# Performance work log

Measured on AMD Instinct MI355X. Metric: run time of the kernel, lower is better.

Reference implementation:

```python
import jax, jax.numpy as jnp
import numpy as np


def setup_inputs() -> dict:
    key = jax.random.key(0)
    k0, k1, k2, k3 = jax.random.split(key, 4)
    B, S, D, F, E = 2, 2048, 1024, 4096, 8
    scale = 0.02
    return {
        "x": jax.random.normal(k0, (B, S, D), jnp.float32),
        "gate_w": jax.random.normal(k1, (E, D), jnp.float32) * scale,
        "gate_b": jnp.zeros((E,), jnp.float32),
        "w1": jax.random.normal(k2, (E, D, F), jnp.float32) * scale,
        "b1": jnp.zeros((E, F), jnp.float32),
        "w2": jax.random.normal(k3, (E, F, D), jnp.float32) * scale,
        "b2": jnp.zeros((E, D), jnp.float32),
        "top_k": 2,
    }


def reference(x, gate_w, gate_b, w1, b1, w2, b2, top_k):
    B, S, D = x.shape
    E = gate_w.shape[0]
    xt = x.reshape(-1, D)                                   # [T, D]
    T = xt.shape[0]

    # Router: softmax over gate logits, then top-k and renormalize.
    gate_probs = jax.nn.softmax(xt @ gate_w.T + gate_b, axis=-1)   # [T, E]
    weights, selected = jax.lax.top_k(gate_probs, top_k)           # [T, k]
    weights = weights / jnp.sum(weights, axis=-1, keepdims=True)

    # Per-token combine weights over experts (zero where not selected),
    # equivalent to the per-expert gather/scatter loop in the original.
    combine = jnp.zeros((T, E), x.dtype).at[
        jnp.arange(T)[:, None], selected
    ].add(weights)                                                 # [T, E]

    # Expert MLPs (dense over experts, masked combine).
    h = jax.nn.silu(jnp.einsum("td,edf->etf", xt, w1) + b1[:, None, :])  # [E, T, F]
    expert_out = jnp.einsum("etf,efd->etd", h, w2) + b2[:, None, :]      # [E, T, D]
    out = jnp.einsum("etd,te->td", expert_out, combine)                  # [T, D]
    return out.reshape(B, S, D)
```

## Files before the change

kernel.cpp:

```cpp
#include <hip/hip_runtime.h>

#define T_TOK 4096
#define DIM   1024
#define FDIM  4096
#define NEXP  8

typedef __bf16 bf16x8 __attribute__((ext_vector_type(8)));
typedef __bf16 bf16x4 __attribute__((ext_vector_type(4)));
typedef float  f32x4  __attribute__((ext_vector_type(4)));
typedef const __attribute__((address_space(3))) char* lds3;

__device__ __forceinline__ void glds16(const void* g, void* l) {
    __builtin_amdgcn_global_load_lds(
        (const __attribute__((address_space(1))) void*)g,
        (__attribute__((address_space(3))) void*)l, 16, 0, 0);
}

#define DSR(dst, a, imm) \
    asm volatile("ds_read_b128 %0, %1 offset:" #imm : "=v"(dst) : "v"(a))

__device__ __forceinline__ int xcd_swz(int phys, int total) {
    int q = total >> 3, r = total & 7;
    int x = phys & 7, i = phys >> 3;
    return (x < r ? x * (q + 1) : r * (q + 1) + (x - r) * q) + i;
}

__global__ __launch_bounds__(64)
void moe_router(const float* __restrict__ x,
                const float* __restrict__ gw,
                const float* __restrict__ gb,
                const int*   __restrict__ topk_p,
                int*   __restrict__ counts,
                int*   __restrict__ bucket,
                float* __restrict__ bweight,
                __bf16* __restrict__ xb) {
    const int t = blockIdx.x;
    const int lane = threadIdx.x;
    float part[NEXP];
#pragma unroll
    for (int e = 0; e < NEXP; ++e) part[e] = 0.f;
    const float* xrow = x + (size_t)t * DIM;
    __bf16* xbrow = xb + (size_t)t * DIM;
#pragma unroll
    for (int r = 0; r < 4; ++r) {
        int c = r * 256 + lane * 4;
        float4 v = *(const float4*)&xrow[c];
        bf16x4 o; o[0]=(__bf16)v.x; o[1]=(__bf16)v.y; o[2]=(__bf16)v.z; o[3]=(__bf16)v.w;
        *(bf16x4*)&xbrow[c] = o;
#pragma unroll
        for (int e = 0; e < NEXP; ++e) {
            float4 g = *(const float4*)&gw[e * DIM + c];
            part[e] += v.x*g.x + v.y*g.y + v.z*g.z + v.w*g.w;
        }
    }
#pragma unroll
    for (int off = 32; off > 0; off >>= 1) {
#pragma unroll
        for (int e = 0; e < NEXP; ++e) part[e] += __shfl_xor(part[e], off);
    }
    if (lane == 0) {
        int k = topk_p[0];
        if (k < 1) k = 1;
        if (k > NEXP) k = NEXP;
        float p[NEXP];
        float mx = -1e30f;
#pragma unroll
        for (int e = 0; e < NEXP; ++e) {
            p[e] = part[e] + gb[e];
            mx = fmaxf(mx, p[e]);
        }
#pragma unroll
        for (int e = 0; e < NEXP; ++e) p[e] = __expf(p[e] - mx);
        bool used[NEXP];
#pragma unroll
        for (int e = 0; e < NEXP; ++e) used[e] = false;
        int sel[NEXP]; float selp[NEXP]; float wsum = 0.f;
        for (int j = 0; j < k; ++j) {
            int best = 0; float bv = -1.f;
            for (int e = 0; e < NEXP; ++e)
                if (!used[e] && p[e] > bv) { bv = p[e]; best = e; }
            used[best] = true; sel[j] = best; selp[j] = bv; wsum += bv;
        }
        for (int j = 0; j < k; ++j) {
            int e = sel[j];
            int pos = atomicAdd(&counts[e], 1);
            bucket[e * T_TOK + pos]  = t;
            bweight[e * T_TOK + pos] = selp[j] / wsum;
        }
    }
}

__global__ __launch_bounds__(256)
void transpose_cvt(const float* __restrict__ in, __bf16* __restrict__ out,
                   int R, int C) {
    const size_t zo = (size_t)blockIdx.z * R * C;
    in += zo; out += zo;
    __shared__ float ts[64][129];
    const int r0 = blockIdx.x * 128, c0 = blockIdx.y * 64;
    const int t = threadIdx.x;
    const int rr = t >> 4;
    const int cl = (t & 15) * 4;
    float4 v[8];
#pragma unroll
    for (int p = 0; p < 8; ++p)
        v[p] = *(const float4*)&in[(size_t)(r0 + p * 16 + rr) * C + c0 + cl];
#pragma unroll
    for (int p = 0; p < 8; ++p) {
        ts[cl + 0][p * 16 + rr] = v[p].x;
        ts[cl + 1][p * 16 + rr] = v[p].y;
        ts[cl + 2][p * 16 + rr] = v[p].z;
        ts[cl + 3][p * 16 + rr] = v[p].w;
    }
    __syncthreads();
    const int oc = t >> 4;
    const int orc = (t & 15) * 8;
#pragma unroll
    for (int p = 0; p < 4; ++p) {
        bf16x8 o;
#pragma unroll
        for (int j = 0; j < 8; ++j) o[j] = (__bf16)ts[p * 16 + oc][orc + j];
        *(bf16x8*)&out[(size_t)(c0 + p * 16 + oc) * R + r0 + orc] = o;
    }
}

__global__ __launch_bounds__(64)
void build_work(const int* __restrict__ counts, int* __restrict__ hdr) {
    __shared__ int off1[NEXP + 1];
    const int lane = threadIdx.x;
    if (lane == 0) {
        int a = 0;
        for (int e = 0; e < NEXP; ++e) {
            off1[e] = a;
            a += (counts[e] + 127) >> 7;
        }
        off1[NEXP] = a;
        hdr[0] = a;
    }
    __syncthreads();
    for (int e = 0; e < NEXP; ++e) {
        int n1 = off1[e + 1] - off1[e];
        for (int j = lane; j < n1; j += 64) hdr[8 + off1[e] + j] = (e << 16) | j;
    }
}

#define STAGE(DST, KO) do { \
    glds16(pA0 + (KO), (DST)); \
    glds16(pA1 + (KO), (DST) + 1024); \
    glds16(pB0 + (KO), (DST) + 8192); \
    glds16(pB1 + (KO), (DST) + 9216); } while (0)

#define PHASE(APTR, BPTR) do { \
    bf16x8 af[4], bfr[4]; \
    DSR(af[0], (APTR), 0);    DSR(af[1], (APTR), 1024); \
    DSR(af[2], (APTR), 2048); DSR(af[3], (APTR), 3072); \
    DSR(bfr[0], (BPTR), 0);    DSR(bfr[1], (BPTR), 1024); \
    DSR(bfr[2], (BPTR), 2048); DSR(bfr[3], (BPTR), 3072); \
    asm volatile("s_waitcnt lgkmcnt(0)"); \
    __builtin_amdgcn_sched_barrier(0); \
    __builtin_amdgcn_s_setprio(1); \
    _Pragma("unroll") for (int i_ = 0; i_ < 4; ++i_) \
    _Pragma("unroll") for (int j_ = 0; j_ < 4; ++j_) \
        acc[i_][j_] = __builtin_amdgcn_mfma_f32_16x16x32_bf16( \
            af[i_], bfr[j_], acc[i_][j_], 0, 0, 0); \
    __builtin_amdgcn_s_setprio(0); \
    __builtin_amdgcn_sched_barrier(0); \
    __syncthreads(); } while (0)

#define KLOOP2(NT) do { \
    STAGE(stg0, 0); \
    __syncthreads(); \
    _Pragma("unroll 1") \
    for (int t_ = 0; t_ < (NT); t_ += 2) { \
        STAGE(stg1, (t_ + 1) * 32); \
        PHASE(aP0, bP0); \
        if (t_ + 2 < (NT)) STAGE(stg0, (t_ + 2) * 32); \
        PHASE(aP1, bP1); \
    } } while (0)

#define GEMM_LANES \
    const int tid = threadIdx.x; \
    const int wave = tid >> 6, lane = tid & 63; \
    const int wm = wave & 1, wn = wave >> 1; \
    const int quad = lane >> 4, l15 = lane & 15; \
    const int lrow = lane >> 2; \
    const int lk8  = (lane & 3) * 8; \
    char* stg0 = sb + wave * 2048; \
    char* stg1 = stg0 + 16384; \
    lds3 s3 = (lds3)sb; \
    lds3 aP0 = s3 + (wm * 64 + l15) * 64 + quad * 16; \
    lds3 bP0 = s3 + 8192 + (wn * 64 + l15) * 64 + quad * 16; \
    lds3 aP1 = aP0 + 16384; \
    lds3 bP1 = bP0 + 16384;

__global__ __launch_bounds__(256, 4)
void moe_gemm1(const __bf16* __restrict__ xb,
               const __bf16* __restrict__ w1t,
               const float*  __restrict__ b1,
               const int*    __restrict__ counts,
               const int*    __restrict__ bucket,
               const int*    __restrict__ hdr,
               __bf16* __restrict__ H) {
    __shared__ __align__(16) char sb[32768];
    __shared__ int tok_s[128];
    GEMM_LANES

    const int n1 = hdr[0];
    const int total = n1 * (FDIM / 128);
    for (int phys = blockIdx.x; phys < total; phys += gridDim.x) {
        const int u = xcd_swz(phys, total);
        const int entry = hdr[8 + (u % n1)];
        const int e = entry >> 16, tile = entry & 0xffff;
        const int nb = (u / n1) * 128;
        const int cnt = counts[e];
        if (tid < 128) {
            int r = tile * 128 + tid;
            if (r >= cnt) r = cnt - 1;
            tok_s[tid] = bucket[e * T_TOK + r];
        }
        __syncthreads();

        const int ar0 = wave * 32 + lrow;
        const __bf16* pA0 = xb + (size_t)tok_s[ar0]      * DIM + lk8;
        const __bf16* pA1 = xb + (size_t)tok_s[ar0 + 16] * DIM + lk8;
        const __bf16* pB0 = w1t + ((size_t)e * FDIM + nb + wave * 32 + lrow) * DIM + lk8;
        const __bf16* pB1 = pB0 + (size_t)16 * DIM;

        f32x4 acc[4][4];
#pragma unroll
        for (int i = 0; i < 4; ++i)
#pragma unroll
            for (int j = 0; j < 4; ++j) acc[i][j] = (f32x4){0.f,0.f,0.f,0.f};

        KLOOP2(DIM / 32);

        __bf16* stg = (__bf16*)(sb + wave * 2304);
        const float* b1e = b1 + e * FDIM + nb + wn * 64;
#pragma unroll
        for (int i = 0; i < 4; ++i) {
#pragma unroll
            for (int j = 0; j < 4; ++j) {
                float bias = b1e[j * 16 + l15];
#pragma unroll
                for (int r = 0; r < 4; ++r) {
                    float v = acc[i][j][r] + bias;
                    float s = v / (1.f + __expf(-v));
                    stg[(quad*4 + r) * 72 + j*16 + l15] = (__bf16)s;
                }
            }
            int prow = tile * 128 + wm * 64 + i * 16 + lrow;
            if (prow < cnt) {
                bf16x8 v0 = *(const bf16x8*)&stg[lrow * 72 + (lane & 3) * 16];
                bf16x8 v1 = *(const bf16x8*)&stg[lrow * 72 + (lane & 3) * 16 + 8];
                __bf16* dst = H + (size_t)(e * T_TOK + prow) * FDIM
                              + nb + wn * 64 + (lane & 3) * 16;
                *(bf16x8*)dst = v0;
                *(bf16x8*)(dst + 8) = v1;
            }
        }
        __syncthreads();
    }
}

#define KSPLIT 2
#define KHALF  (FDIM / KSPLIT)

__global__ __launch_bounds__(256, 4)
void moe_gemm2(const __bf16* __restrict__ H,
               const __bf16* __restrict__ w2t,
               const float*  __restrict__ b2,
               const int*    __restrict__ counts,
               const int*    __restrict__ bucket,
               const float*  __restrict__ bweight,
               const int*    __restrict__ hdr,
               float* __restrict__ out) {
    __shared__ __align__(16) char sb[32768];
    __shared__ int   tok_s[128];
    __shared__ float w_s[128];
    GEMM_LANES

    const int n1 = hdr[0];
    const int total = n1 * (DIM / 128) * KSPLIT;
    for (int phys = blockIdx.x; phys < total; phys += gridDim.x) {
        const int u = xcd_swz(phys, total);
        const int entry = hdr[8 + (u % n1)];
        const int e = entry >> 16, tile = entry & 0xffff;
        const int rest = u / n1;
        const int nb = (rest & 7) * 128;
        const int kc = rest >> 3;
        const int cnt = counts[e];
        if (tid < 128) {
            int r  = tile * 128 + tid;
            int rc = r < cnt ? r : cnt - 1;
            tok_s[tid] = bucket[e * T_TOK + rc];
            w_s[tid]   = bweight[e * T_TOK + rc];
        }
        __syncthreads();

        const size_t kbase = (size_t)kc * KHALF;
        const __bf16* pA0 = H + (size_t)(e * T_TOK + tile * 128 + wave * 32 + lrow) * FDIM
                              + kbase + lk8;
        const __bf16* pA1 = pA0 + (size_t)16 * FDIM;
        const __bf16* pB0 = w2t + ((size_t)e * DIM + nb + wave * 32 + lrow) * FDIM
                              + kbase + lk8;
        const __bf16* pB1 = pB0 + (size_t)16 * FDIM;

        f32x4 acc[4][4];
#pragma unroll
        for (int i = 0; i < 4; ++i)
#pragma unroll
            for (int j = 0; j < 4; ++j) acc[i][j] = (f32x4){0.f,0.f,0.f,0.f};

        KLOOP2(KHALF / 32);

#pragma unroll
        for (int i = 0; i < 4; ++i)
#pragma unroll
            for (int j = 0; j < 4; ++j)
#pragma unroll
                for (int r = 0; r < 4; ++r) {
                    int m = wm*64 + i*16 + quad*4 + r;
                    int prow = tile * 128 + m;
                    if (prow < cnt) {
                        int dc = nb + wn*64 + j*16 + l15;
                        float v = acc[i][j][r] + (kc == 0 ? b2[e * DIM + dc] : 0.f);
                        atomicAdd(&out[(size_t)tok_s[m] * DIM + dc], w_s[m] * v);
                    }
                }
        __syncthreads();
    }
}

extern "C" void kernel_launch(void* const* d_in, const int* in_sizes, int n_in,
                              void* d_out, int out_size, void* d_ws, size_t ws_size,
                              hipStream_t stream) {
    const float* x  = (const float*)d_in[0];
    const float* gw = (const float*)d_in[1];
    const float* gb = (const float*)d_in[2];
    const float* w1 = (const float*)d_in[3];
    const float* b1 = (const float*)d_in[4];
    const float* w2 = (const float*)d_in[5];
    const float* b2 = (const float*)d_in[6];
    const int* topk = (const int*)d_in[7];
    float* out = (float*)d_out;

    char* ws = (char*)d_ws;
    size_t off = 0;
    int* counts = (int*)(ws + off);    off += 256;
    int* bucket = (int*)(ws + off);    off += (size_t)NEXP * T_TOK * 4;
    float* bw   = (float*)(ws + off);  off += (size_t)NEXP * T_TOK * 4;
    int* hdr    = (int*)(ws + off);    off += 4096;
    off = (off + 255) & ~(size_t)255;
    __bf16* xb  = (__bf16*)(ws + off); off += (size_t)T_TOK * DIM * 2;
    __bf16* w1t = (__bf16*)(ws + off); off += (size_t)NEXP * DIM * FDIM * 2;
    __bf16* w2t = (__bf16*)(ws + off); off += (size_t)NEXP * FDIM * DIM * 2;
    __bf16* H   = (__bf16*)(ws + off);

    hipMemsetAsync(counts, 0, 256, stream);
    hipMemsetAsync(out, 0, (size_t)out_size * 4, stream);

    moe_router<<<T_TOK, 64, 0, stream>>>(x, gw, gb, topk, counts, bucket, bw, xb);
    transpose_cvt<<<dim3(DIM/128, FDIM/64, NEXP), 256, 0, stream>>>(w1, w1t, DIM, FDIM);
    transpose_cvt<<<dim3(FDIM/128, DIM/64, NEXP), 256, 0, stream>>>(w2, w2t, FDIM, DIM);
    build_work<<<1, 64, 0, stream>>>(counts, hdr);

    moe_gemm1<<<2048, 256, 0, stream>>>(xb, w1t, b1, counts, bucket, hdr, H);
    moe_gemm2<<<1024, 256, 0, stream>>>(H, w2t, b2, counts, bucket, bw, hdr, out);
}
```

Measured before the change: 720.6 us.

## Enlarge MoE GEMM tiles to 256x128 with 512-thread blocks

Both expert GEMMs move from 128x128 tiles on 256 threads to 256x128 tiles on 8 waves. Each wave now computes 128x32 (8x2 MFMA accumulators), and the LDS staging is resized to 24 KB per buffer. The aim is to halve the weight-tile reloads per token row and raise arithmetic intensity. The cost is more padding waste in partial tiles, since expert counts are now rounded up to 256, and fewer tiles available to fill the GPU.

Measured after the change: 724.0 us. Within noise of the previous version (+0.5%).

```diff
diff --git a/kernel.cpp b/kernel.cpp
--- a/kernel.cpp
+++ b/kernel.cpp
@@ -4,6 +4,7 @@
 #define DIM   1024
 #define FDIM  4096
 #define NEXP  8
+#define BUFSZ 24576
 
 typedef __bf16 bf16x8 __attribute__((ext_vector_type(8)));
 typedef __bf16 bf16x4 __attribute__((ext_vector_type(4)));
@@ -131,7 +132,7 @@
         int a = 0;
         for (int e = 0; e < NEXP; ++e) {
             off1[e] = a;
-            a += (counts[e] + 127) >> 7;
+            a += (counts[e] + 255) >> 8;
         }
         off1[NEXP] = a;
         hdr[0] = a;
@@ -144,22 +145,22 @@
 }
 
 #define STAGE(DST, KO) do { \
-    glds16(pA0 + (KO), (DST)); \
-    glds16(pA1 + (KO), (DST) + 1024); \
-    glds16(pB0 + (KO), (DST) + 8192); \
-    glds16(pB1 + (KO), (DST) + 9216); } while (0)
+    glds16(pA0 + (KO), (DST) + wave * 1024); \
+    glds16(pA1 + (KO), (DST) + 8192 + wave * 1024); \
+    glds16(pB0 + (KO), (DST) + 16384 + wave * 1024); } while (0)
 
 #define PHASE(APTR, BPTR) do { \
-    bf16x8 af[4], bfr[4]; \
+    bf16x8 af[8], bfr[2]; \
     DSR(af[0], (APTR), 0);    DSR(af[1], (APTR), 1024); \
     DSR(af[2], (APTR), 2048); DSR(af[3], (APTR), 3072); \
-    DSR(bfr[0], (BPTR), 0);    DSR(bfr[1], (BPTR), 1024); \
-    DSR(bfr[2], (BPTR), 2048); DSR(bfr[3], (BPTR), 3072); \
+    DSR(af[4], (APTR), 4096); DSR(af[5], (APTR), 5120); \
+    DSR(af[6], (APTR), 6144); DSR(af[7], (APTR), 7168); \
+    DSR(bfr[0], (BPTR), 0);   DSR(bfr[1], (BPTR), 1024); \
     asm volatile("s_waitcnt lgkmcnt(0)"); \
     __builtin_amdgcn_sched_barrier(0); \
     __builtin_amdgcn_s_setprio(1); \
-    _Pragma("unroll") for (int i_ = 0; i_ < 4; ++i_) \
-    _Pragma("unroll") for (int j_ = 0; j_ < 4; ++j_) \
+    _Pragma("unroll") for (int i_ = 0; i_ < 8; ++i_) \
+    _Pragma("unroll") for (int j_ = 0; j_ < 2; ++j_) \
         acc[i_][j_] = __builtin_amdgcn_mfma_f32_16x16x32_bf16( \
             af[i_], bfr[j_], acc[i_][j_], 0, 0, 0); \
     __builtin_amdgcn_s_setprio(0); \
@@ -180,19 +181,20 @@
 #define GEMM_LANES \
     const int tid = threadIdx.x; \
     const int wave = tid >> 6, lane = tid & 63; \
-    const int wm = wave & 1, wn = wave >> 1; \
+    const int wm = wave >> 2, wn = wave & 3;    \
     const int quad = lane >> 4, l15 = lane & 15; \
     const int lrow = lane >> 2; \
     const int lk8  = (lane & 3) * 8; \
-    char* stg0 = sb + wave * 2048; \
-    char* stg1 = stg0 + 16384; \
+    const int srow = (wave << 4) + lrow;        \
+    char* stg0 = sb; \
+    char* stg1 = sb + BUFSZ; \
     lds3 s3 = (lds3)sb; \
-    lds3 aP0 = s3 + (wm * 64 + l15) * 64 + quad * 16; \
-    lds3 bP0 = s3 + 8192 + (wn * 64 + l15) * 64 + quad * 16; \
-    lds3 aP1 = aP0 + 16384; \
-    lds3 bP1 = bP0 + 16384;
-
-__global__ __launch_bounds__(256, 4)
+    lds3 aP0 = s3 + (wm * 128 + l15) * 64 + quad * 16; \
+    lds3 bP0 = s3 + 16384 + (wn * 32 + l15) * 64 + quad * 16; \
+    lds3 aP1 = aP0 + BUFSZ; \
+    lds3 bP1 = bP0 + BUFSZ;
+
+__global__ __launch_bounds__(512, 4)
 void moe_gemm1(const __bf16* __restrict__ xb,
                const __bf16* __restrict__ w1t,
                const float*  __restrict__ b1,
@@ -200,8 +202,8 @@
                const int*    __restrict__ bucket,
                const int*    __restrict__ hdr,
                __bf16* __restrict__ H) {
-    __shared__ __align__(16) char sb[32768];
-    __shared__ int tok_s[128];
+    __shared__ __align__(16) char sb[2 * BUFSZ];
+    __shared__ int tok_s[256];
     GEMM_LANES
 
     const int n1 = hdr[0];
@@ -212,49 +214,45 @@
         const int e = entry >> 16, tile = entry & 0xffff;
         const int nb = (u / n1) * 128;
         const int cnt = counts[e];
-        if (tid < 128) {
-            int r = tile * 128 + tid;
+        if (tid < 256) {
+            int r = tile * 256 + tid;
             if (r >= cnt) r = cnt - 1;
             tok_s[tid] = bucket[e * T_TOK + r];
         }
         __syncthreads();
 
-        const int ar0 = wave * 32 + lrow;
-        const __bf16* pA0 = xb + (size_t)tok_s[ar0]      * DIM + lk8;
-        const __bf16* pA1 = xb + (size_t)tok_s[ar0 + 16] * DIM + lk8;
-        const __bf16* pB0 = w1t + ((size_t)e * FDIM + nb + wave * 32 + lrow) * DIM + lk8;
-        const __bf16* pB1 = pB0 + (size_t)16 * DIM;
-
-        f32x4 acc[4][4];
-#pragma unroll
-        for (int i = 0; i < 4; ++i)
-#pragma unroll
-            for (int j = 0; j < 4; ++j) acc[i][j] = (f32x4){0.f,0.f,0.f,0.f};
+        const __bf16* pA0 = xb + (size_t)tok_s[srow]       * DIM + lk8;
+        const __bf16* pA1 = xb + (size_t)tok_s[srow + 128] * DIM + lk8;
+        const __bf16* pB0 = w1t + ((size_t)e * FDIM + nb + srow) * DIM + lk8;
+
+        f32x4 acc[8][2];
+#pragma unroll
+        for (int i = 0; i < 8; ++i)
+#pragma unroll
+            for (int j = 0; j < 2; ++j) acc[i][j] = (f32x4){0.f,0.f,0.f,0.f};
 
         KLOOP2(DIM / 32);
 
-        __bf16* stg = (__bf16*)(sb + wave * 2304);
-        const float* b1e = b1 + e * FDIM + nb + wn * 64;
-#pragma unroll
-        for (int i = 0; i < 4; ++i) {
-#pragma unroll
-            for (int j = 0; j < 4; ++j) {
+        __bf16* stg = (__bf16*)(sb + wave * 1280);
+        const float* b1e = b1 + e * FDIM + nb + wn * 32;
+#pragma unroll
+        for (int i = 0; i < 8; ++i) {
+#pragma unroll
+            for (int j = 0; j < 2; ++j) {
                 float bias = b1e[j * 16 + l15];
 #pragma unroll
                 for (int r = 0; r < 4; ++r) {
                     float v = acc[i][j][r] + bias;
                     float s = v / (1.f + __expf(-v));
-                    stg[(quad*4 + r) * 72 + j*16 + l15] = (__bf16)s;
+                    stg[(quad*4 + r) * 40 + j*16 + l15] = (__bf16)s;
                 }
             }
-            int prow = tile * 128 + wm * 64 + i * 16 + lrow;
+            int prow = tile * 256 + wm * 128 + i * 16 + lrow;
             if (prow < cnt) {
-                bf16x8 v0 = *(const bf16x8*)&stg[lrow * 72 + (lane & 3) * 16];
-                bf16x8 v1 = *(const bf16x8*)&stg[lrow * 72 + (lane & 3) * 16 + 8];
+                bf16x8 v0 = *(const bf16x8*)&stg[lrow * 40 + (lane & 3) * 8];
                 __bf16* dst = H + (size_t)(e * T_TOK + prow) * FDIM
-                              + nb + wn * 64 + (lane & 3) * 16;
+                              + nb + wn * 32 + (lane & 3) * 8;
                 *(bf16x8*)dst = v0;
-                *(bf16x8*)(dst + 8) = v1;
             }
         }
         __syncthreads();
@@ -264,7 +262,7 @@
 #define KSPLIT 2
 #define KHALF  (FDIM / KSPLIT)
 
-__global__ __launch_bounds__(256, 4)
+__global__ __launch_bounds__(512, 4)
 void moe_gemm2(const __bf16* __restrict__ H,
                const __bf16* __restrict__ w2t,
                const float*  __restrict__ b2,
@@ -273,9 +271,9 @@
                const float*  __restrict__ bweight,
                const int*    __restrict__ hdr,
                float* __restrict__ out) {
-    __shared__ __align__(16) char sb[32768];
-    __shared__ int   tok_s[128];
-    __shared__ float w_s[128];
+    __shared__ __align__(16) char sb[2 * BUFSZ];
+    __shared__ int   tok_s[256];
+    __shared__ float w_s[256];
     GEMM_LANES
 
     const int n1 = hdr[0];
@@ -288,8 +286,8 @@
         const int nb = (rest & 7) * 128;
         const int kc = rest >> 3;
         const int cnt = counts[e];
-        if (tid < 128) {
-            int r  = tile * 128 + tid;
+        if (tid < 256) {
+            int r  = tile * 256 + tid;
             int rc = r < cnt ? r : cnt - 1;
             tok_s[tid] = bucket[e * T_TOK + rc];
             w_s[tid]   = bweight[e * T_TOK + rc];
@@ -297,31 +295,30 @@
         __syncthreads();
 
         const size_t kbase = (size_t)kc * KHALF;
-        const __bf16* pA0 = H + (size_t)(e * T_TOK + tile * 128 + wave * 32 + lrow) * FDIM
+        const __bf16* pA0 = H + (size_t)(e * T_TOK + tile * 256 + srow) * FDIM
                               + kbase + lk8;
-        const __bf16* pA1 = pA0 + (size_t)16 * FDIM;
-        const __bf16* pB0 = w2t + ((size_t)e * DIM + nb + wave * 32 + lrow) * FDIM
+        const __bf16* pA1 = pA0 + (size_t)128 * FDIM;
+        const __bf16* pB0 = w2t + ((size_t)e * DIM + nb + srow) * FDIM
                               + kbase + lk8;
-        const __bf16* pB1 = pB0 + (size_t)16 * FDIM;
-
-        f32x4 acc[4][4];
-#pragma unroll
-        for (int i = 0; i < 4; ++i)
-#pragma unroll
-            for (int j = 0; j < 4; ++j) acc[i][j] = (f32x4){0.f,0.f,0.f,0.f};
+
+        f32x4 acc[8][2];
+#pragma unroll
+        for (int i = 0; i < 8; ++i)
+#pragma unroll
+            for (int j = 0; j < 2; ++j) acc[i][j] = (f32x4){0.f,0.f,0.f,0.f};
 
         KLOOP2(KHALF / 32);
 
 #pragma unroll
-        for (int i = 0; i < 4; ++i)
-#pragma unroll
-            for (int j = 0; j < 4; ++j)
+        for (int i = 0; i < 8; ++i)
+#pragma unroll
+            for (int j = 0; j < 2; ++j)
 #pragma unroll
                 for (int r = 0; r < 4; ++r) {
-                    int m = wm*64 + i*16 + quad*4 + r;
-                    int prow = tile * 128 + m;
+                    int m = wm*128 + i*16 + quad*4 + r;
+                    int prow = tile * 256 + m;
                     if (prow < cnt) {
-                        int dc = nb + wn*64 + j*16 + l15;
+                        int dc = nb + wn*32 + j*16 + l15;
                         float v = acc[i][j][r] + (kc == 0 ? b2[e * DIM + dc] : 0.f);
                         atomicAdd(&out[(size_t)tok_s[m] * DIM + dc], w_s[m] * v);
                     }
@@ -363,6 +360,6 @@
     transpose_cvt<<<dim3(FDIM/128, DIM/64, NEXP), 256, 0, stream>>>(w2, w2t, FDIM, DIM);
     build_work<<<1, 64, 0, stream>>>(counts, hdr);
 
-    moe_gemm1<<<2048, 256, 0, stream>>>(xb, w1t, b1, counts, bucket, hdr, H);
-    moe_gemm2<<<1024, 256, 0, stream>>>(H, w2t, b2, counts, bucket, bw, hdr, out);
-}
+    moe_gemm1<<<1024, 512, 0, stream>>>(xb, w1t, b1, counts, bucket, hdr, H);
+    moe_gemm2<<<512, 512, 0, stream>>>(H, w2t, b2, counts, bucket, bw, hdr, out);
+}
```
